# Performance work log

Measured on AMD Instinct MI355X. Metric: run time of the kernel, lower is better.

## Reference

```python
import jax, jax.numpy as jnp
import numpy as np
import math

B, NQ, NK, D, H = 4, 2048, 2048, 1024, 8
EPS = 1e-5


def _layernorm(x, g, b):
    mu = jnp.mean(x, axis=-1, keepdims=True)
    var = jnp.mean(jnp.square(x - mu), axis=-1, keepdims=True)
    return (x - mu) * jax.lax.rsqrt(var + EPS) * g + b


def setup_inputs() -> dict:
    key = jax.random.key(0)
    ks = jax.random.split(key, 12)
    s = 0.02
    return {
        "q": jax.random.normal(ks[0], (B, NQ, D), jnp.float32),
        "k": jax.random.normal(ks[1], (B, NK, D), jnp.float32),
        "v": jax.random.normal(ks[2], (B, NK, D), jnp.float32),
        "mask": jax.random.randint(ks[3], (B, NK), 0, 2).astype(bool),
        "Wq": jax.random.normal(ks[4], (D, D), jnp.float32) * s,
        "Wk": jax.random.normal(ks[5], (D, D), jnp.float32) * s,
        "Wv": jax.random.normal(ks[6], (D, D), jnp.float32) * s,
        "Wout": jax.random.normal(ks[7], (D, D), jnp.float32) * s,
        "bout": jnp.zeros((D,), jnp.float32),
        "g1": jnp.ones((D,), jnp.float32),
        "b1": jnp.zeros((D,), jnp.float32),
        "g2": jnp.ones((D,), jnp.float32),
        "b2": jnp.zeros((D,), jnp.float32),
    }


def reference(q, k, v, mask, Wq, Wk, Wv, Wout, bout, g1, b1, g2, b2):
    Dh = D // H
    qp = q @ Wq.T  # [B,NQ,D]
    kp = k @ Wk.T  # [B,NK,D]
    vp = v @ Wv.T  # [B,NK,D]
    # scatter: chunk last dim into H heads, cat along batch == reshape to heads
    qh = qp.reshape(B, NQ, H, Dh)
    kh = kp.reshape(B, NK, H, Dh)
    vh = vp.reshape(B, NK, H, Dh)
    # NOTE: original scales by sqrt(dim_out), not sqrt(head_dim)
    logits = jnp.einsum("bqhd,bkhd->bhqk", qh, kh) / math.sqrt(D)
    logits = jnp.where(mask[:, None, None, :], -jnp.inf, logits)
    A = jax.nn.softmax(logits, axis=-1)
    A = jnp.where(jnp.isnan(A), 0.0, A)  # rows fully masked -> 0
    att = jnp.einsum("bhqk,bkhd->bqhd", A, vh).reshape(B, NQ, D)
    out = _layernorm(qp + att, g1, b1)
    out = _layernorm(out + jax.nn.relu(out @ Wout.T + bout), g2, b2)
    return out
```

## Files before the change

### kernel.cpp

```cpp
#include <hip/hip_runtime.h>


typedef __attribute__((ext_vector_type(4))) float f32x4;
typedef __attribute__((ext_vector_type(16))) float f32x16;
typedef __attribute__((ext_vector_type(8))) short s16x8;
typedef __attribute__((ext_vector_type(4))) short s16x4;
typedef __attribute__((ext_vector_type(4))) unsigned int u32x4;

__device__ __forceinline__ unsigned short f2bf(float f) {
  union { float f; unsigned u; } x; x.f = f;
  unsigned r = x.u + 0x7fffu + ((x.u >> 16) & 1u);
  return (unsigned short)(r >> 16);
}
__device__ __forceinline__ float bf2f(unsigned short h) {
  union { unsigned u; float f; } x; x.u = ((unsigned)h) << 16;
  return x.f;
}

__device__ __forceinline__ void gload_lds16(const void* g, void* l) {
  __builtin_amdgcn_global_load_lds(
      (const __attribute__((address_space(1))) unsigned int*)g,
      (__attribute__((address_space(3))) unsigned int*)l, 16, 0, 0);
}

__device__ __forceinline__ unsigned lds_off(const void* p) {
  return (unsigned)(size_t)(const __attribute__((address_space(3))) void*)p;
}

__global__ __launch_bounds__(256) void cvt_w(
    const float* __restrict__ W0, const float* __restrict__ W1,
    const float* __restrict__ W2, const float* __restrict__ W3,
    unsigned short* __restrict__ W0d, unsigned short* __restrict__ W1d,
    unsigned short* __restrict__ W2d, unsigned short* __restrict__ W3d) {
  int i = blockIdx.x * blockDim.x + threadIdx.x;
  const int wsel = i >> 18;
  const float* s = wsel == 0 ? W0 : wsel == 1 ? W1 : wsel == 2 ? W2 : W3;
  unsigned short* d = wsel == 0 ? W0d : wsel == 1 ? W1d : wsel == 2 ? W2d : W3d;
  i &= 262143;
  float4 f = reinterpret_cast<const float4*>(s)[i];
  s16x4 o;
  o[0] = (short)f2bf(f.x); o[1] = (short)f2bf(f.y);
  o[2] = (short)f2bf(f.z); o[3] = (short)f2bf(f.w);
  reinterpret_cast<s16x4*>(d)[i] = o;
}

__device__ __forceinline__ void xcd_tile(int wg, int& brow, int& bcol) {
  const int xcd = wg & 7, idx = wg >> 3;
  brow = ((xcd << 3) + (idx & 7)) * 128;
  bcol = (idx >> 3) * 128;
}

template<int RELU_BIAS>
__global__ __launch_bounds__(256) void gemm_bt(
    const unsigned short* __restrict__ A, const unsigned short* __restrict__ B,
    unsigned short* __restrict__ C, const float* __restrict__ bias,
    int M, int N, int K) {
  __shared__ __align__(16) unsigned short As[128 * 32];
  __shared__ __align__(16) unsigned short Bs[128 * 32];
  const int tid = threadIdx.x;
  const int lane = tid & 63;
  const int w = tid >> 6;
  int brow, bcol;
  xcd_tile(blockIdx.x + (blockIdx.y << 6), brow, bcol);
  const int wr = (w >> 1) * 64;
  const int wc = (w & 1) * 64;

  f32x4 acc[4][4] = {};

  const int srow = w * 32 + (lane >> 2);
  const int scol = (lane & 3) * 8;
  const int rfrag = lane & 15;
  const int kfrag = (lane >> 4) * 8;

  for (int k0 = 0; k0 < K; k0 += 32) {
    __syncthreads();
#pragma unroll
    for (int j = 0; j < 2; ++j) {
      const unsigned short* ga = A + (size_t)(brow + srow + j * 16) * K + k0 + scol;
      gload_lds16(ga, As + (w * 1024 + j * 512));
      const unsigned short* gb = B + (size_t)(bcol + srow + j * 16) * K + k0 + scol;
      gload_lds16(gb, Bs + (w * 1024 + j * 512));
    }
    asm volatile("s_waitcnt vmcnt(0)" ::: "memory");
    __syncthreads();
    s16x8 a[4], b[4];
#pragma unroll
    for (int m = 0; m < 4; ++m)
      a[m] = *(const s16x8*)(As + (wr + m * 16 + rfrag) * 32 + kfrag);
#pragma unroll
    for (int n = 0; n < 4; ++n)
      b[n] = *(const s16x8*)(Bs + (wc + n * 16 + rfrag) * 32 + kfrag);
#pragma unroll
    for (int m = 0; m < 4; ++m)
#pragma unroll
      for (int n = 0; n < 4; ++n)
        acc[m][n] = __builtin_amdgcn_mfma_f32_16x16x32_bf16(a[m], b[n], acc[m][n], 0, 0, 0);
  }

  const int crow = brow + wr + ((lane >> 4) * 4);
  const int ccol = bcol + wc + (lane & 15);
  float bv[4];
  if (RELU_BIAS) {
#pragma unroll
    for (int n = 0; n < 4; ++n) bv[n] = bias[ccol + n * 16];
  }
#pragma unroll
  for (int m = 0; m < 4; ++m)
#pragma unroll
    for (int n = 0; n < 4; ++n)
#pragma unroll
      for (int r = 0; r < 4; ++r) {
        float vv = acc[m][n][r];
        if (RELU_BIAS) vv = fmaxf(vv + bv[n], 0.f);
        C[(size_t)(crow + m * 16 + r) * N + ccol + n * 16] = f2bf(vv);
      }
}

__global__ __launch_bounds__(256) void gemm_proj3(
    const float* __restrict__ A0, const float* __restrict__ A1,
    const float* __restrict__ A2, const unsigned short* __restrict__ B0,
    const unsigned short* __restrict__ B1, const unsigned short* __restrict__ B2,
    unsigned short* __restrict__ C0, unsigned short* __restrict__ C1,
    unsigned short* __restrict__ C2, int M, int N, int K) {
  const int z = blockIdx.z;
  const float* __restrict__ A = z == 0 ? A0 : z == 1 ? A1 : A2;
  const unsigned short* __restrict__ B = z == 0 ? B0 : z == 1 ? B1 : B2;
  unsigned short* __restrict__ C = z == 0 ? C0 : z == 1 ? C1 : C2;

  __shared__ __align__(16) float Asf[128 * 32];
  __shared__ __align__(16) unsigned short Bs[128 * 32];
  const int tid = threadIdx.x;
  const int lane = tid & 63;
  const int w = tid >> 6;
  int brow, bcol;
  xcd_tile(blockIdx.x + (blockIdx.y << 6), brow, bcol);
  const int wr = (w >> 1) * 64;
  const int wc = (w & 1) * 64;

  f32x4 acc[4][4] = {};

  const int srow = w * 32 + (lane >> 2);
  const int scol = (lane & 3) * 8;
  const int arow = w * 32 + (lane >> 3);
  const int acb = (lane & 7) * 16;
  const int rfrag = lane & 15;
  const int quad = lane >> 4;

  for (int k0 = 0; k0 < K; k0 += 32) {
    __syncthreads();
#pragma unroll
    for (int j = 0; j < 2; ++j) {
      const unsigned short* gb = B + (size_t)(bcol + srow + j * 16) * K + k0 + scol;
      gload_lds16(gb, Bs + (w * 1024 + j * 512));
    }
#pragma unroll
    for (int j = 0; j < 4; ++j) {
      int row = arow + j * 8;
      int cbs = acb ^ ((row & 7) << 4);
      const float* ga = A + (size_t)(brow + row) * K + k0 + (cbs >> 2);
      gload_lds16(ga, (char*)Asf + w * 4096 + j * 1024);
    }
    asm volatile("s_waitcnt vmcnt(0)" ::: "memory");
    __syncthreads();
    s16x8 a[4], b[4];
#pragma unroll
    for (int m = 0; m < 4; ++m) {
      const int r = wr + m * 16 + rfrag;
      const int b1 = (quad * 32) ^ ((r & 7) << 4);
      const int b2 = (quad * 32 + 16) ^ ((r & 7) << 4);
      f32x4 a0 = *(const f32x4*)((const char*)Asf + r * 128 + b1);
      f32x4 a1 = *(const f32x4*)((const char*)Asf + r * 128 + b2);
      unsigned w0, w1, w2, w3;
      asm("v_cvt_pk_bf16_f32 %0, %1, %2" : "=v"(w0) : "v"(a0[0]), "v"(a0[1]));
      asm("v_cvt_pk_bf16_f32 %0, %1, %2" : "=v"(w1) : "v"(a0[2]), "v"(a0[3]));
      asm("v_cvt_pk_bf16_f32 %0, %1, %2" : "=v"(w2) : "v"(a1[0]), "v"(a1[1]));
      asm("v_cvt_pk_bf16_f32 %0, %1, %2" : "=v"(w3) : "v"(a1[2]), "v"(a1[3]));
      u32x4 wv; wv[0] = w0; wv[1] = w1; wv[2] = w2; wv[3] = w3;
      a[m] = *(s16x8*)&wv;
    }
#pragma unroll
    for (int n = 0; n < 4; ++n)
      b[n] = *(const s16x8*)(Bs + (wc + n * 16 + rfrag) * 32 + quad * 8);
#pragma unroll
    for (int m = 0; m < 4; ++m)
#pragma unroll
      for (int n = 0; n < 4; ++n)
        acc[m][n] = __builtin_amdgcn_mfma_f32_16x16x32_bf16(a[m], b[n], acc[m][n], 0, 0, 0);
  }

  const int crow = brow + wr + (quad * 4);
  const int ccol = bcol + wc + rfrag;
#pragma unroll
  for (int m = 0; m < 4; ++m)
#pragma unroll
    for (int n = 0; n < 4; ++n)
#pragma unroll
      for (int r = 0; r < 4; ++r)
        C[(size_t)(crow + m * 16 + r) * N + ccol + n * 16] = f2bf(acc[m][n][r]);
}

__global__ __launch_bounds__(256, 2) void attn_fused(
    const unsigned short* __restrict__ Qp, const unsigned short* __restrict__ Kp,
    const unsigned short* __restrict__ Vp, const int* __restrict__ mask,
    unsigned short* __restrict__ Att) {
  constexpr int DD = 1024, NK = 2048;
  __shared__ __align__(16) unsigned short lds[16384];
  __shared__ __align__(16) float smaskF[2048];
  unsigned short* Ks = lds;
  unsigned short* Vs = lds + 8192;

  const int tid = threadIdx.x, lane = tid & 63, w = tid >> 6;
  const int quad = lane >> 4, lq = lane & 15;
  const int hi = lane >> 5, q5 = lane & 31;
  const int L = blockIdx.x;
  const int bh = (L & 7) * 4 + (L >> 7);
  const int qt = (L >> 3) & 15;
  const int b = bh >> 3, h = bh & 7;
  const int q0 = qt * 128;
  const unsigned short* Qbase = Qp + ((size_t)b * 2048 + q0) * DD + h * 128;
  const unsigned short* Kbase = Kp + (size_t)b * 2048 * DD + h * 128;
  const unsigned short* Vbase = Vp + (size_t)b * 2048 * DD + h * 128;

#pragma unroll
  for (int j = 0; j < 8; ++j) {
    int row = w * 32 + j * 4 + quad;
    const unsigned short* g = Qbase + (size_t)row * DD + lq * 8;
    gload_lds16(g, lds + w * 4096 + j * 512);
  }
  asm volatile("s_waitcnt vmcnt(0)" ::: "memory");
  __syncthreads();
  s16x8 qf[8];
#pragma unroll
  for (int ds = 0; ds < 8; ++ds)
    qf[ds] = *(const s16x8*)(lds + (w * 32 + q5) * 128 + ds * 16 + hi * 8);

  {
    const int4* mp = (const int4*)(mask + b * NK);
    int4 m0 = mp[tid];
    int4 m1 = mp[tid + 256];
    f32x4 w0, w1;
    w0[0] = m0.x ? -1e30f : 0.f; w0[1] = m0.y ? -1e30f : 0.f;
    w0[2] = m0.z ? -1e30f : 0.f; w0[3] = m0.w ? -1e30f : 0.f;
    w1[0] = m1.x ? -1e30f : 0.f; w1[1] = m1.y ? -1e30f : 0.f;
    w1[2] = m1.z ? -1e30f : 0.f; w1[3] = m1.w ? -1e30f : 0.f;
    *(f32x4*)(smaskF + 4 * tid) = w0;
    *(f32x4*)(smaskF + 4 * (tid + 256)) = w1;
  }

  const unsigned vb0 = lds_off(Vs);
  const int swzq = (q5 & 7) << 4;

  f32x16 o[4] = {};
  float mrow = -1e30f, lrow = 0.f;

  for (int kt = 0; kt < NK / 64; ++kt) {
    const int k0 = kt * 64;
    __syncthreads();
#pragma unroll
    for (int j = 0; j < 4; ++j) {
      int row = w * 16 + j * 4 + quad;
      int cb = lq * 16;
      int cbs = cb ^ ((row & 7) << 4);
      const unsigned short* g = Kbase + (size_t)(k0 + row) * DD + (cbs >> 1);
      gload_lds16(g, Ks + w * 2048 + j * 512);
    }
#pragma unroll
    for (int it = 0; it < 4; ++it) {
      int s = w * 256 + it * 64 + lane;
      int kk = ((s >> 6) << 2) | ((s >> 1) & 3);
      int dd = (((s >> 3) & 7) << 4) | ((s & 1) << 3);
      const unsigned short* g = Vbase + (size_t)(k0 + kk) * DD + dd;
      gload_lds16(g, Vs + (size_t)(w * 256 + it * 64) * 8);
    }
    asm volatile("s_waitcnt vmcnt(0)" ::: "memory");
    __syncthreads();

    f32x16 acc0 = {}, acc1 = {};
    __builtin_amdgcn_s_setprio(1);
#pragma unroll
    for (int ds = 0; ds < 8; ++ds) {
      int cbs = (ds * 32 + hi * 16) ^ swzq;
      s16x8 kf0 = *(const s16x8*)((const char*)Ks + q5 * 256 + cbs);
      s16x8 kf1 = *(const s16x8*)((const char*)Ks + (q5 + 32) * 256 + cbs);
      acc0 = __builtin_amdgcn_mfma_f32_32x32x16_bf16(kf0, qf[ds], acc0, 0, 0, 0);
      acc1 = __builtin_amdgcn_mfma_f32_32x32x16_bf16(kf1, qf[ds], acc1, 0, 0, 0);
    }
    __builtin_amdgcn_s_setprio(0);

    float sv0[16], sv1[16];
#pragma unroll
    for (int g2 = 0; g2 < 4; ++g2) {
      f32x4 m0 = *(const f32x4*)(smaskF + k0 + g2 * 8 + hi * 4);
      f32x4 m1 = *(const f32x4*)(smaskF + k0 + 32 + g2 * 8 + hi * 4);
#pragma unroll
      for (int j2 = 0; j2 < 4; ++j2) {
        sv0[g2 * 4 + j2] = fmaf(acc0[g2 * 4 + j2], 0.03125f, m0[j2]);
        sv1[g2 * 4 + j2] = fmaf(acc1[g2 * 4 + j2], 0.03125f, m1[j2]);
      }
    }

    float tm = fmaxf(sv0[0], sv1[0]);
#pragma unroll
    for (int r = 1; r < 16; ++r) tm = fmaxf(tm, fmaxf(sv0[r], sv1[r]));
    tm = fmaxf(tm, __shfl_xor(tm, 32, 64));
    const bool up = !__all(tm - mrow <= 8.f);
    float al = 1.f;
    if (up) {
      float mn = fmaxf(mrow, tm);
      al = __expf(mrow - mn);
      mrow = mn;
    }
    float rs = 0.f;
    s16x8 pa[4];
    auto packP = [&](const float (&sv)[16], s16x8* paOut) {
      float p[16];
#pragma unroll
      for (int r = 0; r < 16; ++r) {
        p[r] = __expf(sv[r] - mrow);
        rs += p[r];
      }
#pragma unroll
      for (int i2 = 0; i2 < 2; ++i2) {
        unsigned a0, b0, a1, b1;
        asm("v_cvt_pk_bf16_f32 %0, %1, %2" : "=v"(a0) : "v"(p[i2 * 8 + 0]), "v"(p[i2 * 8 + 1]));
        asm("v_cvt_pk_bf16_f32 %0, %1, %2" : "=v"(b0) : "v"(p[i2 * 8 + 4]), "v"(p[i2 * 8 + 5]));
        asm("v_cvt_pk_bf16_f32 %0, %1, %2" : "=v"(a1) : "v"(p[i2 * 8 + 2]), "v"(p[i2 * 8 + 3]));
        asm("v_cvt_pk_bf16_f32 %0, %1, %2" : "=v"(b1) : "v"(p[i2 * 8 + 6]), "v"(p[i2 * 8 + 7]));
        asm volatile("v_permlane32_swap_b32 %0, %1" : "+v"(a0), "+v"(b0));
        asm volatile("v_permlane32_swap_b32 %0, %1" : "+v"(a1), "+v"(b1));
        u32x4 wv;
        wv[0] = a0; wv[1] = a1; wv[2] = b0; wv[3] = b1;
        paOut[i2] = *(s16x8*)&wv;
      }
    };
    packP(sv0, &pa[0]);
    packP(sv1, &pa[2]);
    rs += __shfl_xor(rs, 32, 64);
    lrow = lrow * al + rs;
    if (up) {
#pragma unroll
      for (int reg = 0; reg < 16; ++reg) {
        float alo = __shfl(al, (reg & 3) + 8 * (reg >> 2) + 4 * hi, 64);
#pragma unroll
        for (int db = 0; db < 4; ++db) o[db][reg] *= alo;
      }
    }

#pragma unroll
    for (int db = 0; db < 4; ++db) {
      s16x4 vlo[4], vhi[4];
#pragma unroll
      for (int kb2 = 0; kb2 < 4; ++kb2) {
        const unsigned va = vb0 + (kb2 * 4 + hi * 2) * 1024 +
                            (db * 2 + (quad & 1)) * 128 + lq * 8;
        asm volatile("ds_read_b64_tr_b16 %0, %2\n\t"
                     "ds_read_b64_tr_b16 %1, %2 offset:1024"
                     : "=&v"(vlo[kb2]), "=&v"(vhi[kb2])
                     : "v"(va)
                     : "memory");
      }
      asm volatile("s_waitcnt lgkmcnt(0)" ::: "memory");
      __builtin_amdgcn_sched_barrier(0);
      __builtin_amdgcn_s_setprio(1);
#pragma unroll
      for (int kb2 = 0; kb2 < 4; ++kb2) {
        s16x8 vv;
#pragma unroll
        for (int j = 0; j < 4; ++j) { vv[j] = vlo[kb2][j]; vv[4 + j] = vhi[kb2][j]; }
        o[db] = __builtin_amdgcn_mfma_f32_32x32x16_bf16(pa[kb2], vv, o[db], 0, 0, 0);
      }
      __builtin_amdgcn_s_setprio(0);
    }
  }

  float inv = (mrow <= -1e29f || lrow <= 0.f) ? 0.f : 1.f / lrow;
#pragma unroll
  for (int reg = 0; reg < 16; ++reg) {
    const int rown = (reg & 3) + 8 * (reg >> 2) + 4 * hi;
    float invo = __shfl(inv, rown, 64);
    const int q = q0 + w * 32 + rown;
#pragma unroll
    for (int db = 0; db < 4; ++db) {
      Att[((size_t)b * 2048 + q) * DD + h * 128 + db * 32 + q5] =
          f2bf(o[db][reg] * invo);
    }
  }
}

template<int OUT_F32>
__global__ __launch_bounds__(256) void add_ln(
    const unsigned short* __restrict__ X, const unsigned short* __restrict__ Y,
    const float* __restrict__ gam, const float* __restrict__ bet,
    void* __restrict__ out) {
  const int row = blockIdx.x;
  const int tid = threadIdx.x;
  const int lane = tid & 63, w = tid >> 6;
  __shared__ float rbuf[8];
  const size_t base = (size_t)row * 1024 + tid * 4;
  s16x4 xa = *(const s16x4*)(X + base);
  s16x4 yb = *(const s16x4*)(Y + base);
  float x[4];
  float s1 = 0.f, s2 = 0.f;
#pragma unroll
  for (int j = 0; j < 4; ++j) {
    x[j] = bf2f((unsigned short)xa[j]) + bf2f((unsigned short)yb[j]);
    s1 += x[j];
    s2 += x[j] * x[j];
  }
#pragma unroll
  for (int d = 1; d < 64; d <<= 1) {
    s1 += __shfl_xor(s1, d, 64);
    s2 += __shfl_xor(s2, d, 64);
  }
  if (lane == 0) { rbuf[w] = s1; rbuf[4 + w] = s2; }
  __syncthreads();
  float t1 = rbuf[0] + rbuf[1] + rbuf[2] + rbuf[3];
  float t2 = rbuf[4] + rbuf[5] + rbuf[6] + rbuf[7];
  float mu = t1 * (1.f / 1024.f);
  float var = t2 * (1.f / 1024.f) - mu * mu;
  float rstd = rsqrtf(fmaxf(var, 0.f) + 1e-5f);
  float4 g4 = *(const float4*)(gam + tid * 4);
  float4 b4 = *(const float4*)(bet + tid * 4);
  float gg[4] = {g4.x, g4.y, g4.z, g4.w};
  float bb[4] = {b4.x, b4.y, b4.z, b4.w};
  if (OUT_F32) {
    float4 o4;
    o4.x = (x[0] - mu) * rstd * gg[0] + bb[0];
    o4.y = (x[1] - mu) * rstd * gg[1] + bb[1];
    o4.z = (x[2] - mu) * rstd * gg[2] + bb[2];
    o4.w = (x[3] - mu) * rstd * gg[3] + bb[3];
    *(float4*)((float*)out + base) = o4;
  } else {
    s16x4 o;
#pragma unroll
    for (int j = 0; j < 4; ++j)
      o[j] = (short)f2bf((x[j] - mu) * rstd * gg[j] + bb[j]);
    *(s16x4*)((unsigned short*)out + base) = o;
  }
}

extern "C" void kernel_launch(void* const* d_in, const int* in_sizes, int n_in,
                              void* d_out, int out_size, void* d_ws, size_t ws_size,
                              hipStream_t stream) {
  const float* q  = (const float*)d_in[0];
  const float* k  = (const float*)d_in[1];
  const float* v  = (const float*)d_in[2];
  const int* msk  = (const int*)d_in[3];
  const float* Wq = (const float*)d_in[4];
  const float* Wk = (const float*)d_in[5];
  const float* Wv = (const float*)d_in[6];
  const float* Wo = (const float*)d_in[7];
  const float* bo = (const float*)d_in[8];
  const float* g1 = (const float*)d_in[9];
  const float* b1 = (const float*)d_in[10];
  const float* g2 = (const float*)d_in[11];
  const float* b2 = (const float*)d_in[12];
  float* out = (float*)d_out;

  char* ws = (char*)d_ws;
  const size_t S = (size_t)8192 * 1024 * 2;
  unsigned short* qpb = (unsigned short*)(ws + 3 * S);
  unsigned short* kpb = (unsigned short*)(ws + 4 * S);
  unsigned short* vpb = (unsigned short*)(ws + 5 * S);
  unsigned short* attb = (unsigned short*)(ws + 0 * S);
  unsigned short* h1b  = (unsigned short*)(ws + 1 * S);
  unsigned short* h2b  = (unsigned short*)(ws + 2 * S);
  unsigned short* Wqb = (unsigned short*)(ws + 6 * S);
  unsigned short* Wkb = Wqb + (size_t)1024 * 1024;
  unsigned short* Wvb = Wkb + (size_t)1024 * 1024;
  unsigned short* Wob = Wvb + (size_t)1024 * 1024;

  cvt_w<<<4096, 256, 0, stream>>>(Wq, Wk, Wv, Wo, Wqb, Wkb, Wvb, Wob);

  gemm_proj3<<<dim3(64, 8, 3), 256, 0, stream>>>(
      q, k, v, Wqb, Wkb, Wvb, qpb, kpb, vpb, 8192, 1024, 1024);

  attn_fused<<<512, 256, 0, stream>>>(qpb, kpb, vpb, msk, attb);

  add_ln<0><<<8192, 256, 0, stream>>>(qpb, attb, g1, b1, (void*)h1b);
  gemm_bt<1><<<dim3(64, 8), 256, 0, stream>>>(h1b, Wob, h2b, bo, 8192, 1024, 1024);
  add_ln<1><<<8192, 256, 0, stream>>>(h1b, h2b, g2, b2, (void*)out);
}
```

Baseline: 228.8 us.

## Double-buffer K/V tiles in LDS to overlap global loads with attention compute

The attention kernel's shared-memory area doubles so K and V tiles have two buffers each. The loads for tile kt+1 are issued into the spare buffer right after the barrier, while tile kt is being computed, instead of loading and waiting at the start of each iteration. This is meant to hide global-to-LDS latency behind the QK and PV MFMA work and drops one barrier per iteration. The cost is twice the LDS per block, which could limit occupancy. The explicit vmcnt wait is also gone, so correctness depends on the compiler inserting waits for the async LDS DMA.

Result: slower. 239.2 us (+4.6%).

```diff
diff --git a/kernel.cpp b/kernel.cpp
--- a/kernel.cpp
+++ b/kernel.cpp
@@ -204,10 +204,8 @@
     const unsigned short* __restrict__ Vp, const int* __restrict__ mask,
     unsigned short* __restrict__ Att) {
   constexpr int DD = 1024, NK = 2048;
-  __shared__ __align__(16) unsigned short lds[16384];
+  __shared__ __align__(16) unsigned short lds[32768];
   __shared__ __align__(16) float smaskF[2048];
-  unsigned short* Ks = lds;
-  unsigned short* Vs = lds + 8192;
 
   const int tid = threadIdx.x, lane = tid & 63, w = tid >> 6;
   const int quad = lane >> 4, lq = lane & 15;
@@ -247,41 +245,57 @@
     *(f32x4*)(smaskF + 4 * (tid + 256)) = w1;
   }
 
-  const unsigned vb0 = lds_off(Vs);
-  const int swzq = (q5 & 7) << 4;
-
-  f32x16 o[4] = {};
-  float mrow = -1e30f, lrow = 0.f;
-
-  for (int kt = 0; kt < NK / 64; ++kt) {
-    const int k0 = kt * 64;
-    __syncthreads();
+  auto stageK = [&](int t, int bsel) {
+    const int kk0 = t * 64;
 #pragma unroll
     for (int j = 0; j < 4; ++j) {
       int row = w * 16 + j * 4 + quad;
       int cb = lq * 16;
       int cbs = cb ^ ((row & 7) << 4);
-      const unsigned short* g = Kbase + (size_t)(k0 + row) * DD + (cbs >> 1);
-      gload_lds16(g, Ks + w * 2048 + j * 512);
-    }
+      const unsigned short* g = Kbase + (size_t)(kk0 + row) * DD + (cbs >> 1);
+      gload_lds16(g, lds + bsel * 8192 + w * 2048 + j * 512);
+    }
+  };
+  auto stageV = [&](int t, int bsel) {
+    const int kk0 = t * 64;
 #pragma unroll
     for (int it = 0; it < 4; ++it) {
       int s = w * 256 + it * 64 + lane;
       int kk = ((s >> 6) << 2) | ((s >> 1) & 3);
       int dd = (((s >> 3) & 7) << 4) | ((s & 1) << 3);
-      const unsigned short* g = Vbase + (size_t)(k0 + kk) * DD + dd;
-      gload_lds16(g, Vs + (size_t)(w * 256 + it * 64) * 8);
-    }
-    asm volatile("s_waitcnt vmcnt(0)" ::: "memory");
+      const unsigned short* g = Vbase + (size_t)(kk0 + kk) * DD + dd;
+      gload_lds16(g, lds + 16384 + bsel * 8192 + w * 2048 + it * 512);
+    }
+  };
+
+  __syncthreads();
+  stageK(0, 0);
+  stageV(0, 0);
+
+  const unsigned vb00 = lds_off(lds + 16384);
+  const int swzq = (q5 & 7) << 4;
+
+  f32x16 o[4] = {};
+  float mrow = -1e30f, lrow = 0.f;
+
+  for (int kt = 0; kt < NK / 64; ++kt) {
+    const int k0 = kt * 64;
+    const int cur = kt & 1;
     __syncthreads();
+    if (kt < NK / 64 - 1) {
+      stageK(kt + 1, cur ^ 1);
+      stageV(kt + 1, cur ^ 1);
+    }
+    const char* Kc = (const char*)lds + cur * 16384;
+    const unsigned vbase = vb00 + cur * 16384;
 
     f32x16 acc0 = {}, acc1 = {};
     __builtin_amdgcn_s_setprio(1);
 #pragma unroll
     for (int ds = 0; ds < 8; ++ds) {
       int cbs = (ds * 32 + hi * 16) ^ swzq;
-      s16x8 kf0 = *(const s16x8*)((const char*)Ks + q5 * 256 + cbs);
-      s16x8 kf1 = *(const s16x8*)((const char*)Ks + (q5 + 32) * 256 + cbs);
+      s16x8 kf0 = *(const s16x8*)(Kc + q5 * 256 + cbs);
+      s16x8 kf1 = *(const s16x8*)(Kc + (q5 + 32) * 256 + cbs);
       acc0 = __builtin_amdgcn_mfma_f32_32x32x16_bf16(kf0, qf[ds], acc0, 0, 0, 0);
       acc1 = __builtin_amdgcn_mfma_f32_32x32x16_bf16(kf1, qf[ds], acc1, 0, 0, 0);
     }
@@ -351,7 +365,7 @@
       s16x4 vlo[4], vhi[4];
 #pragma unroll
       for (int kb2 = 0; kb2 < 4; ++kb2) {
-        const unsigned va = vb0 + (kb2 * 4 + hi * 2) * 1024 +
+        const unsigned va = vbase + (kb2 * 4 + hi * 2) * 1024 +
                             (db * 2 + (quad & 1)) * 128 + lq * 8;
         asm volatile("ds_read_b64_tr_b16 %0, %2\n\t"
                      "ds_read_b64_tr_b16 %1, %2 offset:1024"
```
